# Optimization experiments

Measured on AMD Instinct MI355X. Metric: run time of the kernel, lower is better.

The kernel has to match this reference:

```python
import jax, jax.numpy as jnp
import numpy as np

EMBED_DIM = 768
NUM_HEADS = 12
HEAD_DIM = EMBED_DIM // NUM_HEADS
B, T = 2, 2048


def setup_inputs() -> dict:
    key = jax.random.key(0)
    ks = jax.random.split(key, 11)
    s = 1.0 / np.sqrt(EMBED_DIM)
    return {
        "query": jax.random.normal(ks[0], (B, T, EMBED_DIM), jnp.float32),
        "key_in": jax.random.normal(ks[1], (B, T, EMBED_DIM), jnp.float32),
        "value": jax.random.normal(ks[2], (B, T, EMBED_DIM), jnp.float32),
        "Wq": jax.random.uniform(ks[3], (EMBED_DIM, EMBED_DIM), jnp.float32, -s, s),
        "bq": jnp.zeros((EMBED_DIM,), jnp.float32),
        "Wk": jax.random.uniform(ks[4], (EMBED_DIM, EMBED_DIM), jnp.float32, -s, s),
        "bk": jnp.zeros((EMBED_DIM,), jnp.float32),
        "Wv": jax.random.uniform(ks[5], (EMBED_DIM, EMBED_DIM), jnp.float32, -s, s),
        "bv": jnp.zeros((EMBED_DIM,), jnp.float32),
        "Wo": jax.random.uniform(ks[6], (EMBED_DIM, EMBED_DIM), jnp.float32, -s, s),
        "bo": jnp.zeros((EMBED_DIM,), jnp.float32),
    }


def reference(query, key_in, value, Wq, bq, Wk, bk, Wv, bv, Wo, bo):
    b, t, _ = query.shape

    def split_heads(x):  # [B,T,E] -> [B,H,T,Dh]
        return x.reshape(b, t, NUM_HEADS, HEAD_DIM).transpose(0, 2, 1, 3)

    Q = split_heads(query @ Wq + bq)
    K = split_heads(key_in @ Wk + bk)
    V = split_heads(value @ Wv + bv)

    scores = jnp.einsum("bhqd,bhkd->bhqk", Q, K) / np.sqrt(HEAD_DIM).astype(np.float32)
    attn = jax.nn.softmax(scores, axis=-1)
    out = jnp.einsum("bhqk,bhkd->bhqd", attn, V)  # [B,H,T,Dh]
    out = out.transpose(0, 2, 1, 3).reshape(b, t, EMBED_DIM)
    return out @ Wo + bo
```

## Files before the change

kernel.cpp:

```cpp
#include <hip/hip_runtime.h>
#include <math.h>

typedef __attribute__((ext_vector_type(4))) float  floatx4;
typedef __attribute__((ext_vector_type(16))) float f32x16;
typedef __attribute__((ext_vector_type(8))) short  short8;
typedef __attribute__((ext_vector_type(4))) short  short4v;
typedef __attribute__((ext_vector_type(8))) __bf16 bf16x8;
typedef __attribute__((ext_vector_type(4))) unsigned int uint4v;

#define E_DIM 768
#define T_DIM 2048
#define N_B   2
#define N_H   12
#define H_D   64
#define M_TOT 4096

#define Q_SCALE 0.1803368801111204f

#if __has_builtin(__builtin_amdgcn_exp2f)
#define EXP2F(x) __builtin_amdgcn_exp2f(x)
#else
#define EXP2F(x) exp2f(x)
#endif
#if __has_builtin(__builtin_amdgcn_rcpf)
#define RCPF(x) __builtin_amdgcn_rcpf(x)
#else
#define RCPF(x) (1.0f / (x))
#endif

__device__ __forceinline__ unsigned short f32_to_bf16(float f) {
  unsigned int u = __float_as_uint(f);
  u += 0x7fffu + ((u >> 16) & 1u);
  return (unsigned short)(u >> 16);
}

__device__ __forceinline__ void lds_barrier() {
  asm volatile("s_waitcnt lgkmcnt(0)\n\ts_barrier" ::: "memory");
}

__device__ __forceinline__ void gload_lds16(const unsigned short* g, unsigned short* l) {
  __builtin_amdgcn_global_load_lds(
      (const __attribute__((address_space(1))) unsigned int*)(const void*)g,
      (__attribute__((address_space(3))) unsigned int*)(void*)l, 16, 0, 0);
}

__device__ __forceinline__ unsigned int cvtpk_bf16(float lo, float hi) {
  unsigned int r;
  asm("v_cvt_pk_bf16_f32 %0, %1, %2" : "=v"(r) : "v"(lo), "v"(hi));
  return r;
}

__device__ __forceinline__ void perml32_swap(unsigned int& a, unsigned int& b) {
  asm volatile("v_permlane32_swap_b32 %0, %1" : "+v"(a), "+v"(b));
}

__global__ __launch_bounds__(256) void convert_x(const float* __restrict__ q,
                                                 const float* __restrict__ k,
                                                 const float* __restrict__ v,
                                                 unsigned short* __restrict__ Xb) {
  const int z = blockIdx.y;
  const float* src = (z == 0) ? q : (z == 1) ? k : v;
  size_t idx = ((size_t)blockIdx.x * 256 + threadIdx.x) * 4;
  float4 val = *reinterpret_cast<const float4*>(&src[idx]);
  short4v o;
  o[0] = (short)f32_to_bf16(val.x);
  o[1] = (short)f32_to_bf16(val.y);
  o[2] = (short)f32_to_bf16(val.z);
  o[3] = (short)f32_to_bf16(val.w);
  *reinterpret_cast<short4v*>(&Xb[(size_t)z * M_TOT * E_DIM + idx]) = o;
}

__global__ __launch_bounds__(256) void transpose_w4(const float* __restrict__ W0,
                                                    const float* __restrict__ W1,
                                                    const float* __restrict__ W2,
                                                    const float* __restrict__ W3,
                                                    unsigned short* __restrict__ Wt) {
  __shared__ float tile[32][33];
  const int z = blockIdx.z;
  const float* W = (z == 0) ? W0 : (z == 1) ? W1 : (z == 2) ? W2 : W3;
  unsigned short* dst = Wt + (size_t)z * E_DIM * E_DIM;
  int k0 = blockIdx.x * 32, n0 = blockIdx.y * 32;
  int tx = threadIdx.x & 31, ty = threadIdx.x >> 5;
  for (int i = 0; i < 4; i++)
    tile[ty + i * 8][tx] = W[(size_t)(k0 + ty + i * 8) * E_DIM + n0 + tx];
  __syncthreads();
  for (int i = 0; i < 4; i++)
    dst[(size_t)(n0 + ty + i * 8) * E_DIM + k0 + tx] = f32_to_bf16(tile[tx][ty + i * 8]);
}

__global__ __launch_bounds__(256) void gemm_qkv(const unsigned short* __restrict__ Xb,
                                                const unsigned short* __restrict__ WtAll,
                                                const float* __restrict__ bq,
                                                const float* __restrict__ bk,
                                                const float* __restrict__ bv,
                                                unsigned short* __restrict__ outQKV) {
  __shared__ unsigned short As[128 * 32];
  __shared__ unsigned short Bs[128 * 32];

  const int z = blockIdx.z;
  const unsigned short* A = Xb + (size_t)z * M_TOT * E_DIM;
  const float* bias = (z == 0) ? bq : (z == 1) ? bk : bv;
  const unsigned short* W = WtAll + (size_t)z * E_DIM * E_DIM;
  unsigned short* out = outQKV + (size_t)z * M_TOT * E_DIM;
  const float scale = (z == 0) ? Q_SCALE : 1.0f;

  const int tid = threadIdx.x;
  const int lane = tid & 63, wv = tid >> 6;
  const int m15 = lane & 15, quad = lane >> 4;
  const int wm = (wv & 1) * 64, wn = (wv >> 1) * 64;
  const int m0 = blockIdx.x * 128, n0 = blockIdx.y * 128;

  floatx4 acc[4][4] = {};
  const int srow = lane >> 2, scol = (lane & 3) * 8;

  for (int k0 = 0; k0 < E_DIM; k0 += 32) {
    for (int cc = 0; cc < 2; cc++) {
      int c = wv * 2 + cc;
      gload_lds16(&A[(size_t)(m0 + c * 16 + srow) * E_DIM + k0 + scol], &As[c * 512]);
      gload_lds16(&W[(size_t)(n0 + c * 16 + srow) * E_DIM + k0 + scol], &Bs[c * 512]);
    }
    __syncthreads();
    bf16x8 af[4], bfr[4];
    for (int i = 0; i < 4; i++)
      af[i] = *reinterpret_cast<const bf16x8*>(&As[(wm + i * 16 + m15) * 32 + quad * 8]);
    for (int j = 0; j < 4; j++)
      bfr[j] = *reinterpret_cast<const bf16x8*>(&Bs[(wn + j * 16 + m15) * 32 + quad * 8]);
    for (int i = 0; i < 4; i++)
      for (int j = 0; j < 4; j++)
        acc[i][j] = __builtin_amdgcn_mfma_f32_16x16x32_bf16(af[i], bfr[j], acc[i][j], 0, 0, 0);
    __syncthreads();
  }

  for (int i = 0; i < 4; i++)
    for (int j = 0; j < 4; j++) {
      int gn = n0 + wn + j * 16 + m15;
      int h = gn >> 6, d = gn & 63;
      float bso = bias[gn];
      for (int r = 0; r < 4; r++) {
        int gm = m0 + wm + i * 16 + quad * 4 + r;
        int bb = gm >> 11, tt = gm & 2047;
        float v = (acc[i][j][r] + bso) * scale;
        out[(((size_t)bb * N_H + h) * T_DIM + tt) * H_D + d] = f32_to_bf16(v);
      }
    }
}

__global__ __launch_bounds__(256) void transpose_v(const unsigned short* __restrict__ Vg_all,
                                                   unsigned short* __restrict__ VT) {
  __shared__ unsigned short tile[64 * 72];
  const int t0 = blockIdx.x * 64, h = blockIdx.y, bb = blockIdx.z;
  const unsigned short* Vg = Vg_all + (((size_t)bb * N_H + h) * T_DIM) * H_D;
  unsigned short* VTh = VT + (((size_t)bb * N_H + h) * H_D) * T_DIM;
  const int tid = threadIdx.x;
  const int tloc = tid & 63, d0 = (tid >> 6) * 16;

  short8 r0 = *reinterpret_cast<const short8*>(&Vg[(size_t)(t0 + tloc) * H_D + d0]);
  short8 r1 = *reinterpret_cast<const short8*>(&Vg[(size_t)(t0 + tloc) * H_D + d0 + 8]);
#pragma unroll
  for (int j = 0; j < 8; j++) {
    tile[(d0 + j) * 72 + tloc] = (unsigned short)r0[j];
    tile[(d0 + 8 + j) * 72 + tloc] = (unsigned short)r1[j];
  }
  __syncthreads();
  const int d = tid >> 2, ts = (tid & 3) * 16;
  short8 w0 = *reinterpret_cast<const short8*>(&tile[d * 72 + ts]);
  short8 w1 = *reinterpret_cast<const short8*>(&tile[d * 72 + ts + 8]);
  *reinterpret_cast<short8*>(&VTh[(size_t)d * T_DIM + t0 + ts]) = w0;
  *reinterpret_cast<short8*>(&VTh[(size_t)d * T_DIM + t0 + ts + 8]) = w1;
}

__global__ __launch_bounds__(128) void attn(const unsigned short* __restrict__ QKV,
                                            const unsigned short* __restrict__ VT,
                                            unsigned short* __restrict__ ctx) {
  __shared__ unsigned short Ks[2][64 * 64];
  __shared__ unsigned short Vs[2][64 * 64];

  const int qt = blockIdx.x, h = blockIdx.y, bb = blockIdx.z;
  const size_t headoff = (((size_t)bb * N_H + h) * T_DIM) * H_D;
  const unsigned short* Qg = QKV + headoff;
  const unsigned short* Kg = QKV + (size_t)M_TOT * E_DIM + headoff;
  const unsigned short* VTg = VT + (((size_t)bb * N_H + h) * H_D) * T_DIM;

  const int tid = threadIdx.x;
  const int lane = tid & 63, wv = tid >> 6;
  const int l31 = lane & 31, hi = lane >> 5, l7 = lane & 7;
  const int q0 = qt * 64 + wv * 32;

  const int srow = lane >> 3;
  const int sslot = (lane & 7) ^ srow;
  const unsigned short* gK = Kg + (size_t)srow * H_D + sslot * 8;
  const unsigned short* gV = VTg + (size_t)srow * T_DIM + sslot * 8;

  bf16x8 aq[4];
#pragma unroll
  for (int c = 0; c < 4; c++)
    aq[c] = *reinterpret_cast<const bf16x8*>(&Qg[(size_t)(q0 + l31) * H_D + c * 16 + hi * 8]);

#pragma unroll
  for (int i = 0; i < 8; i++) {
    if (wv == 0) gload_lds16(gK + (size_t)(i * 8) * H_D, &Ks[0][i * 512]);
    else         gload_lds16(gV + (size_t)(i * 8) * T_DIM, &Vs[0][i * 512]);
  }
  if (wv == 0) {
#pragma unroll
    for (int i = 0; i < 8; i++)
      gload_lds16(gK + (size_t)(64 + i * 8) * H_D, &Ks[1][i * 512]);
  }
  asm volatile("s_waitcnt vmcnt(0)" ::: "memory");
  lds_barrier();

  f32x16 o0 = {}, o1 = {};
  float lacc = 0.f;
  bf16x8 pa0[2], pa1[2];

  auto QK = [&](const unsigned short* kb, f32x16& s0, f32x16& s1) {
#pragma unroll
    for (int c = 0; c < 4; c++) {
      const int slot = ((c << 1) | hi) ^ l7;
      bf16x8 k0 = *reinterpret_cast<const bf16x8*>(&kb[l31 * 64 + slot * 8]);
      bf16x8 k1 = *reinterpret_cast<const bf16x8*>(&kb[(32 + l31) * 64 + slot * 8]);
      s0 = __builtin_amdgcn_mfma_f32_32x32x16_bf16(k0, aq[c], s0, 0, 0, 0);
      s1 = __builtin_amdgcn_mfma_f32_32x32x16_bf16(k1, aq[c], s1, 0, 0, 0);
    }
  };
  auto PV = [&](const unsigned short* vb) {
#pragma unroll
    for (int cc = 0; cc < 2; cc++) {
      const int sl0 = ((cc << 1) | hi) ^ l7;
      const int sl1 = (4 + (cc << 1) + hi) ^ l7;
      bf16x8 v00 = *reinterpret_cast<const bf16x8*>(&vb[l31 * 64 + sl0 * 8]);
      bf16x8 v01 = *reinterpret_cast<const bf16x8*>(&vb[(32 + l31) * 64 + sl0 * 8]);
      bf16x8 v10 = *reinterpret_cast<const bf16x8*>(&vb[l31 * 64 + sl1 * 8]);
      bf16x8 v11 = *reinterpret_cast<const bf16x8*>(&vb[(32 + l31) * 64 + sl1 * 8]);
      o0 = __builtin_amdgcn_mfma_f32_32x32x16_bf16(pa0[cc], v00, o0, 0, 0, 0);
      o1 = __builtin_amdgcn_mfma_f32_32x32x16_bf16(pa0[cc], v01, o1, 0, 0, 0);
      o0 = __builtin_amdgcn_mfma_f32_32x32x16_bf16(pa1[cc], v10, o0, 0, 0, 0);
      o1 = __builtin_amdgcn_mfma_f32_32x32x16_bf16(pa1[cc], v11, o1, 0, 0, 0);
    }
  };
  auto PACK = [&](f32x16& s0, f32x16& s1) {
#pragma unroll
    for (int i = 0; i < 16; i++) { s0[i] = EXP2F(s0[i]); s1[i] = EXP2F(s1[i]); }
    float a0 = 0.f, a1 = 0.f, a2 = 0.f, a3 = 0.f;
#pragma unroll
    for (int i = 0; i < 16; i += 4) {
      a0 += s0[i]; a1 += s0[i + 1]; a2 += s0[i + 2]; a3 += s0[i + 3];
      a0 += s1[i]; a1 += s1[i + 1]; a2 += s1[i + 2]; a3 += s1[i + 3];
    }
    lacc += (a0 + a1) + (a2 + a3);
#pragma unroll
    for (int cc = 0; cc < 2; cc++) {
      {
        unsigned int x0 = cvtpk_bf16(s0[8 * cc + 0], s0[8 * cc + 1]);
        unsigned int x1 = cvtpk_bf16(s0[8 * cc + 2], s0[8 * cc + 3]);
        unsigned int y0 = cvtpk_bf16(s0[8 * cc + 4], s0[8 * cc + 5]);
        unsigned int y1 = cvtpk_bf16(s0[8 * cc + 6], s0[8 * cc + 7]);
        perml32_swap(x0, y0);
        perml32_swap(x1, y1);
        uint4v u; u[0] = x0; u[1] = x1; u[2] = y0; u[3] = y1;
        pa0[cc] = __builtin_bit_cast(bf16x8, u);
      }
      {
        unsigned int x0 = cvtpk_bf16(s1[8 * cc + 0], s1[8 * cc + 1]);
        unsigned int x1 = cvtpk_bf16(s1[8 * cc + 2], s1[8 * cc + 3]);
        unsigned int y0 = cvtpk_bf16(s1[8 * cc + 4], s1[8 * cc + 5]);
        unsigned int y1 = cvtpk_bf16(s1[8 * cc + 6], s1[8 * cc + 7]);
        perml32_swap(x0, y0);
        perml32_swap(x1, y1);
        uint4v u; u[0] = x0; u[1] = x1; u[2] = y0; u[3] = y1;
        pa1[cc] = __builtin_bit_cast(bf16x8, u);
      }
    }
  };

  {
    f32x16 s0 = {}, s1 = {};
    __builtin_amdgcn_s_setprio(1);
    QK(Ks[0], s0, s1);
    __builtin_amdgcn_s_setprio(0);
    lds_barrier();
#pragma unroll
    for (int i = 0; i < 8; i++) {
      if (wv == 0) gload_lds16(gK + (size_t)(128 + i * 8) * H_D, &Ks[0][i * 512]);
      else         gload_lds16(gV + (size_t)(i * 8) * T_DIM + 64, &Vs[1][i * 512]);
    }
    PACK(s0, s1);
    asm volatile("s_waitcnt vmcnt(8)" ::: "memory");
    lds_barrier();
  }

  for (int kt = 1; kt <= 30; ++kt) {
    f32x16 s0 = {}, s1 = {};
    __builtin_amdgcn_s_setprio(1);
    QK(Ks[kt & 1], s0, s1);
    PV(Vs[(kt - 1) & 1]);
    __builtin_amdgcn_s_setprio(0);
    lds_barrier();
    if (wv == 0) {
      if (kt < 30) {
        const int nt = kt + 2;
#pragma unroll
        for (int i = 0; i < 8; i++)
          gload_lds16(gK + (size_t)(nt * 64 + i * 8) * H_D, &Ks[kt & 1][i * 512]);
      }
    } else {
      const int nt = kt + 1;
#pragma unroll
      for (int i = 0; i < 8; i++)
        gload_lds16(gV + (size_t)(i * 8) * T_DIM + nt * 64, &Vs[nt & 1][i * 512]);
    }
    PACK(s0, s1);
    if (kt == 30) asm volatile("s_waitcnt vmcnt(0)" ::: "memory");
    else          asm volatile("s_waitcnt vmcnt(8)" ::: "memory");
    lds_barrier();
  }

  {
    f32x16 s0 = {}, s1 = {};
    __builtin_amdgcn_s_setprio(1);
    QK(Ks[1], s0, s1);
    PV(Vs[0]);
    __builtin_amdgcn_s_setprio(0);
    PACK(s0, s1);
    __builtin_amdgcn_s_setprio(1);
    PV(Vs[1]);
    __builtin_amdgcn_s_setprio(0);
  }

  float ltot = lacc + __shfl_xor(lacc, 32, 64);
  float rl = RCPF(ltot);
  const size_t obase = ((size_t)bb * T_DIM + q0) * E_DIM + (size_t)h * H_D;
#pragma unroll
  for (int r = 0; r < 16; r++) {
    const int qrow = (r & 3) + 8 * (r >> 2) + 4 * hi;
    float rq = __shfl(rl, qrow, 64);
    ctx[obase + (size_t)qrow * E_DIM + l31]      = f32_to_bf16(o0[r] * rq);
    ctx[obase + (size_t)qrow * E_DIM + 32 + l31] = f32_to_bf16(o1[r] * rq);
  }
}

__global__ __launch_bounds__(256) void gemm_out(const unsigned short* __restrict__ Actx,
                                                const unsigned short* __restrict__ Wt,
                                                const float* __restrict__ bias,
                                                float* __restrict__ out) {
  __shared__ unsigned short As[64 * 32];
  __shared__ unsigned short Bs[128 * 32];

  const int tid = threadIdx.x;
  const int lane = tid & 63, wv = tid >> 6;
  const int m15 = lane & 15, quad = lane >> 4;
  const int wm = (wv & 1) * 32, wn = (wv >> 1) * 64;
  const int m0 = blockIdx.x * 64, n0 = blockIdx.y * 128;

  floatx4 acc[2][4] = {};
  const int srow = lane >> 2, scol = (lane & 3) * 8;

  for (int k0 = 0; k0 < E_DIM; k0 += 32) {
    gload_lds16(&Actx[(size_t)(m0 + wv * 16 + srow) * E_DIM + k0 + scol], &As[wv * 512]);
    for (int cc = 0; cc < 2; cc++) {
      int c = wv * 2 + cc;
      gload_lds16(&Wt[(size_t)(n0 + c * 16 + srow) * E_DIM + k0 + scol], &Bs[c * 512]);
    }
    __syncthreads();
    bf16x8 af[2], bfr[4];
    for (int i = 0; i < 2; i++)
      af[i] = *reinterpret_cast<const bf16x8*>(&As[(wm + i * 16 + m15) * 32 + quad * 8]);
    for (int j = 0; j < 4; j++)
      bfr[j] = *reinterpret_cast<const bf16x8*>(&Bs[(wn + j * 16 + m15) * 32 + quad * 8]);
    for (int i = 0; i < 2; i++)
      for (int j = 0; j < 4; j++)
        acc[i][j] = __builtin_amdgcn_mfma_f32_16x16x32_bf16(af[i], bfr[j], acc[i][j], 0, 0, 0);
    __syncthreads();
  }

  for (int i = 0; i < 2; i++)
    for (int j = 0; j < 4; j++) {
      int gn = n0 + wn + j * 16 + m15;
      float bso = bias[gn];
      for (int r = 0; r < 4; r++) {
        int gm = m0 + wm + i * 16 + quad * 4 + r;
        out[(size_t)gm * E_DIM + gn] = acc[i][j][r] + bso;
      }
    }
}

extern "C" void kernel_launch(void* const* d_in, const int* in_sizes, int n_in,
                              void* d_out, int out_size, void* d_ws, size_t ws_size,
                              hipStream_t stream) {
  const float* query  = (const float*)d_in[0];
  const float* key_in = (const float*)d_in[1];
  const float* value  = (const float*)d_in[2];
  const float* Wq = (const float*)d_in[3];
  const float* bq = (const float*)d_in[4];
  const float* Wk = (const float*)d_in[5];
  const float* bk = (const float*)d_in[6];
  const float* Wv = (const float*)d_in[7];
  const float* bv = (const float*)d_in[8];
  const float* Wo = (const float*)d_in[9];
  const float* bo = (const float*)d_in[10];
  float* out = (float*)d_out;

  unsigned short* ws  = (unsigned short*)d_ws;
  unsigned short* Wt  = ws;
  unsigned short* Xb  = Wt + (size_t)4 * E_DIM * E_DIM;
  unsigned short* QKV = Xb + (size_t)3 * M_TOT * E_DIM;
  unsigned short* VT  = QKV + (size_t)3 * M_TOT * E_DIM;
  unsigned short* ctx = VT + (size_t)N_B * N_H * H_D * T_DIM;

  dim3 tb(256);
  convert_x<<<dim3(M_TOT * E_DIM / 1024, 3), tb, 0, stream>>>(query, key_in, value, Xb);
  transpose_w4<<<dim3(24, 24, 4), tb, 0, stream>>>(Wq, Wk, Wv, Wo, Wt);

  gemm_qkv<<<dim3(32, 6, 3), tb, 0, stream>>>(Xb, Wt, bq, bk, bv, QKV);
  transpose_v<<<dim3(32, 12, 2), tb, 0, stream>>>(QKV + (size_t)2 * M_TOT * E_DIM, VT);
  attn<<<dim3(32, 12, 2), dim3(128), 0, stream>>>(QKV, VT, ctx);
  gemm_out<<<dim3(64, 6), tb, 0, stream>>>(ctx, Wt + (size_t)3 * E_DIM * E_DIM, bo, out);
  (void)in_sizes; (void)n_in; (void)out_size; (void)ws_size;
}
```

Before: 194.6 us.

## Process 64 query rows per single-wave attention block, drop LDS barriers

```diff
diff --git a/kernel.cpp b/kernel.cpp
--- a/kernel.cpp
+++ b/kernel.cpp
@@ -169,9 +169,9 @@
   *reinterpret_cast<short8*>(&VTh[(size_t)d * T_DIM + t0 + ts + 8]) = w1;
 }
 
-__global__ __launch_bounds__(128) void attn(const unsigned short* __restrict__ QKV,
-                                            const unsigned short* __restrict__ VT,
-                                            unsigned short* __restrict__ ctx) {
+__global__ __launch_bounds__(64, 1) void attn(const unsigned short* __restrict__ QKV,
+                                              const unsigned short* __restrict__ VT,
+                                              unsigned short* __restrict__ ctx) {
   __shared__ unsigned short Ks[2][64 * 64];
   __shared__ unsigned short Vs[2][64 * 64];
 
@@ -181,46 +181,48 @@
   const unsigned short* Kg = QKV + (size_t)M_TOT * E_DIM + headoff;
   const unsigned short* VTg = VT + (((size_t)bb * N_H + h) * H_D) * T_DIM;
 
-  const int tid = threadIdx.x;
-  const int lane = tid & 63, wv = tid >> 6;
+  const int lane = threadIdx.x;
   const int l31 = lane & 31, hi = lane >> 5, l7 = lane & 7;
-  const int q0 = qt * 64 + wv * 32;
+  const int q0 = qt * 64;
 
   const int srow = lane >> 3;
   const int sslot = (lane & 7) ^ srow;
   const unsigned short* gK = Kg + (size_t)srow * H_D + sslot * 8;
   const unsigned short* gV = VTg + (size_t)srow * T_DIM + sslot * 8;
 
-  bf16x8 aq[4];
-#pragma unroll
-  for (int c = 0; c < 4; c++)
-    aq[c] = *reinterpret_cast<const bf16x8*>(&Qg[(size_t)(q0 + l31) * H_D + c * 16 + hi * 8]);
+  bf16x8 aqA[4], aqB[4];
+#pragma unroll
+  for (int c = 0; c < 4; c++) {
+    aqA[c] = *reinterpret_cast<const bf16x8*>(&Qg[(size_t)(q0 + l31) * H_D + c * 16 + hi * 8]);
+    aqB[c] = *reinterpret_cast<const bf16x8*>(&Qg[(size_t)(q0 + 32 + l31) * H_D + c * 16 + hi * 8]);
+  }
 
 #pragma unroll
   for (int i = 0; i < 8; i++) {
-    if (wv == 0) gload_lds16(gK + (size_t)(i * 8) * H_D, &Ks[0][i * 512]);
-    else         gload_lds16(gV + (size_t)(i * 8) * T_DIM, &Vs[0][i * 512]);
-  }
-  if (wv == 0) {
-#pragma unroll
-    for (int i = 0; i < 8; i++)
-      gload_lds16(gK + (size_t)(64 + i * 8) * H_D, &Ks[1][i * 512]);
-  }
-  asm volatile("s_waitcnt vmcnt(0)" ::: "memory");
-  lds_barrier();
-
-  f32x16 o0 = {}, o1 = {};
-  float lacc = 0.f;
-  bf16x8 pa0[2], pa1[2];
-
-  auto QK = [&](const unsigned short* kb, f32x16& s0, f32x16& s1) {
+    gload_lds16(gK + (size_t)(i * 8) * H_D, &Ks[0][i * 512]);
+    gload_lds16(gV + (size_t)(i * 8) * T_DIM, &Vs[0][i * 512]);
+  }
+#pragma unroll
+  for (int i = 0; i < 8; i++) {
+    gload_lds16(gK + (size_t)(64 + i * 8) * H_D, &Ks[1][i * 512]);
+    gload_lds16(gV + (size_t)(i * 8) * T_DIM + 64, &Vs[1][i * 512]);
+  }
+  asm volatile("s_waitcnt vmcnt(16)" ::: "memory");
+
+  f32x16 oA0 = {}, oA1 = {}, oB0 = {}, oB1 = {};
+  float laccA = 0.f, laccB = 0.f;
+  bf16x8 paA0[2], paA1[2], paB0[2], paB1[2];
+
+  auto QK = [&](const unsigned short* kb, f32x16& a0, f32x16& a1, f32x16& b0, f32x16& b1) {
 #pragma unroll
     for (int c = 0; c < 4; c++) {
       const int slot = ((c << 1) | hi) ^ l7;
       bf16x8 k0 = *reinterpret_cast<const bf16x8*>(&kb[l31 * 64 + slot * 8]);
       bf16x8 k1 = *reinterpret_cast<const bf16x8*>(&kb[(32 + l31) * 64 + slot * 8]);
-      s0 = __builtin_amdgcn_mfma_f32_32x32x16_bf16(k0, aq[c], s0, 0, 0, 0);
-      s1 = __builtin_amdgcn_mfma_f32_32x32x16_bf16(k1, aq[c], s1, 0, 0, 0);
+      a0 = __builtin_amdgcn_mfma_f32_32x32x16_bf16(k0, aqA[c], a0, 0, 0, 0);
+      a1 = __builtin_amdgcn_mfma_f32_32x32x16_bf16(k1, aqA[c], a1, 0, 0, 0);
+      b0 = __builtin_amdgcn_mfma_f32_32x32x16_bf16(k0, aqB[c], b0, 0, 0, 0);
+      b1 = __builtin_amdgcn_mfma_f32_32x32x16_bf16(k1, aqB[c], b1, 0, 0, 0);
     }
   };
   auto PV = [&](const unsigned short* vb) {
@@ -232,13 +234,17 @@
       bf16x8 v01 = *reinterpret_cast<const bf16x8*>(&vb[(32 + l31) * 64 + sl0 * 8]);
       bf16x8 v10 = *reinterpret_cast<const bf16x8*>(&vb[l31 * 64 + sl1 * 8]);
       bf16x8 v11 = *reinterpret_cast<const bf16x8*>(&vb[(32 + l31) * 64 + sl1 * 8]);
-      o0 = __builtin_amdgcn_mfma_f32_32x32x16_bf16(pa0[cc], v00, o0, 0, 0, 0);
-      o1 = __builtin_amdgcn_mfma_f32_32x32x16_bf16(pa0[cc], v01, o1, 0, 0, 0);
-      o0 = __builtin_amdgcn_mfma_f32_32x32x16_bf16(pa1[cc], v10, o0, 0, 0, 0);
-      o1 = __builtin_amdgcn_mfma_f32_32x32x16_bf16(pa1[cc], v11, o1, 0, 0, 0);
+      oA0 = __builtin_amdgcn_mfma_f32_32x32x16_bf16(paA0[cc], v00, oA0, 0, 0, 0);
+      oA1 = __builtin_amdgcn_mfma_f32_32x32x16_bf16(paA0[cc], v01, oA1, 0, 0, 0);
+      oA0 = __builtin_amdgcn_mfma_f32_32x32x16_bf16(paA1[cc], v10, oA0, 0, 0, 0);
+      oA1 = __builtin_amdgcn_mfma_f32_32x32x16_bf16(paA1[cc], v11, oA1, 0, 0, 0);
+      oB0 = __builtin_amdgcn_mfma_f32_32x32x16_bf16(paB0[cc], v00, oB0, 0, 0, 0);
+      oB1 = __builtin_amdgcn_mfma_f32_32x32x16_bf16(paB0[cc], v01, oB1, 0, 0, 0);
+      oB0 = __builtin_amdgcn_mfma_f32_32x32x16_bf16(paB1[cc], v10, oB0, 0, 0, 0);
+      oB1 = __builtin_amdgcn_mfma_f32_32x32x16_bf16(paB1[cc], v11, oB1, 0, 0, 0);
     }
   };
-  auto PACK = [&](f32x16& s0, f32x16& s1) {
+  auto PACK1 = [&](f32x16& s0, f32x16& s1, float& lacc, bf16x8* pl, bf16x8* ph) {
 #pragma unroll
     for (int i = 0; i < 16; i++) { s0[i] = EXP2F(s0[i]); s1[i] = EXP2F(s1[i]); }
     float a0 = 0.f, a1 = 0.f, a2 = 0.f, a3 = 0.f;
@@ -258,7 +264,7 @@
         perml32_swap(x0, y0);
         perml32_swap(x1, y1);
         uint4v u; u[0] = x0; u[1] = x1; u[2] = y0; u[3] = y1;
-        pa0[cc] = __builtin_bit_cast(bf16x8, u);
+        pl[cc] = __builtin_bit_cast(bf16x8, u);
       }
       {
         unsigned int x0 = cvtpk_bf16(s1[8 * cc + 0], s1[8 * cc + 1]);
@@ -268,74 +274,78 @@
         perml32_swap(x0, y0);
         perml32_swap(x1, y1);
         uint4v u; u[0] = x0; u[1] = x1; u[2] = y0; u[3] = y1;
-        pa1[cc] = __builtin_bit_cast(bf16x8, u);
+        ph[cc] = __builtin_bit_cast(bf16x8, u);
       }
     }
   };
 
   {
-    f32x16 s0 = {}, s1 = {};
+    f32x16 sA0 = {}, sA1 = {}, sB0 = {}, sB1 = {};
     __builtin_amdgcn_s_setprio(1);
-    QK(Ks[0], s0, s1);
+    QK(Ks[0], sA0, sA1, sB0, sB1);
     __builtin_amdgcn_s_setprio(0);
-    lds_barrier();
-#pragma unroll
-    for (int i = 0; i < 8; i++) {
-      if (wv == 0) gload_lds16(gK + (size_t)(128 + i * 8) * H_D, &Ks[0][i * 512]);
-      else         gload_lds16(gV + (size_t)(i * 8) * T_DIM + 64, &Vs[1][i * 512]);
-    }
-    PACK(s0, s1);
+    asm volatile("s_waitcnt lgkmcnt(0)" ::: "memory");
+#pragma unroll
+    for (int i = 0; i < 8; i++)
+      gload_lds16(gK + (size_t)(128 + i * 8) * H_D, &Ks[0][i * 512]);
+    PACK1(sA0, sA1, laccA, paA0, paA1);
+    PACK1(sB0, sB1, laccB, paB0, paB1);
     asm volatile("s_waitcnt vmcnt(8)" ::: "memory");
-    lds_barrier();
   }
 
   for (int kt = 1; kt <= 30; ++kt) {
-    f32x16 s0 = {}, s1 = {};
+    f32x16 sA0 = {}, sA1 = {}, sB0 = {}, sB1 = {};
     __builtin_amdgcn_s_setprio(1);
-    QK(Ks[kt & 1], s0, s1);
+    QK(Ks[kt & 1], sA0, sA1, sB0, sB1);
     PV(Vs[(kt - 1) & 1]);
     __builtin_amdgcn_s_setprio(0);
-    lds_barrier();
-    if (wv == 0) {
-      if (kt < 30) {
-        const int nt = kt + 2;
-#pragma unroll
-        for (int i = 0; i < 8; i++)
-          gload_lds16(gK + (size_t)(nt * 64 + i * 8) * H_D, &Ks[kt & 1][i * 512]);
-      }
-    } else {
-      const int nt = kt + 1;
+    asm volatile("s_waitcnt lgkmcnt(0)" ::: "memory");
+    if (kt < 30) {
+      const int nk = kt + 2;
 #pragma unroll
       for (int i = 0; i < 8; i++)
-        gload_lds16(gV + (size_t)(i * 8) * T_DIM + nt * 64, &Vs[nt & 1][i * 512]);
-    }
-    PACK(s0, s1);
-    if (kt == 30) asm volatile("s_waitcnt vmcnt(0)" ::: "memory");
-    else          asm volatile("s_waitcnt vmcnt(8)" ::: "memory");
-    lds_barrier();
+        gload_lds16(gK + (size_t)(nk * 64 + i * 8) * H_D, &Ks[kt & 1][i * 512]);
+    }
+    {
+      const int nv = kt + 1;
+#pragma unroll
+      for (int i = 0; i < 8; i++)
+        gload_lds16(gV + (size_t)(i * 8) * T_DIM + nv * 64, &Vs[nv & 1][i * 512]);
+    }
+    PACK1(sA0, sA1, laccA, paA0, paA1);
+    PACK1(sB0, sB1, laccB, paB0, paB1);
+    if (kt < 30) asm volatile("s_waitcnt vmcnt(16)" ::: "memory");
+    else         asm volatile("s_waitcnt vmcnt(8)" ::: "memory");
   }
 
   {
-    f32x16 s0 = {}, s1 = {};
+    f32x16 sA0 = {}, sA1 = {}, sB0 = {}, sB1 = {};
     __builtin_amdgcn_s_setprio(1);
-    QK(Ks[1], s0, s1);
+    QK(Ks[1], sA0, sA1, sB0, sB1);
     PV(Vs[0]);
     __builtin_amdgcn_s_setprio(0);
-    PACK(s0, s1);
+    PACK1(sA0, sA1, laccA, paA0, paA1);
+    PACK1(sB0, sB1, laccB, paB0, paB1);
+    asm volatile("s_waitcnt vmcnt(0)" ::: "memory");
     __builtin_amdgcn_s_setprio(1);
     PV(Vs[1]);
     __builtin_amdgcn_s_setprio(0);
   }
 
-  float ltot = lacc + __shfl_xor(lacc, 32, 64);
-  float rl = RCPF(ltot);
+  float ltA = laccA + __shfl_xor(laccA, 32, 64);
+  float rlA = RCPF(ltA);
+  float ltB = laccB + __shfl_xor(laccB, 32, 64);
+  float rlB = RCPF(ltB);
   const size_t obase = ((size_t)bb * T_DIM + q0) * E_DIM + (size_t)h * H_D;
 #pragma unroll
   for (int r = 0; r < 16; r++) {
-    const int qrow = (r & 3) + 8 * (r >> 2) + 4 * hi;
-    float rq = __shfl(rl, qrow, 64);
-    ctx[obase + (size_t)qrow * E_DIM + l31]      = f32_to_bf16(o0[r] * rq);
-    ctx[obase + (size_t)qrow * E_DIM + 32 + l31] = f32_to_bf16(o1[r] * rq);
+    const int qr = (r & 3) + 8 * (r >> 2) + 4 * hi;
+    float ra = __shfl(rlA, qr, 64);
+    ctx[obase + (size_t)qr * E_DIM + l31]      = f32_to_bf16(oA0[r] * ra);
+    ctx[obase + (size_t)qr * E_DIM + 32 + l31] = f32_to_bf16(oA1[r] * ra);
+    float rb = __shfl(rlB, qr, 64);
+    ctx[obase + (size_t)(32 + qr) * E_DIM + l31]      = f32_to_bf16(oB0[r] * rb);
+    ctx[obase + (size_t)(32 + qr) * E_DIM + 32 + l31] = f32_to_bf16(oB1[r] * rb);
   }
 }
 
@@ -413,7 +423,7 @@
 
   gemm_qkv<<<dim3(32, 6, 3), tb, 0, stream>>>(Xb, Wt, bq, bk, bv, QKV);
   transpose_v<<<dim3(32, 12, 2), tb, 0, stream>>>(QKV + (size_t)2 * M_TOT * E_DIM, VT);
-  attn<<<dim3(32, 12, 2), dim3(128), 0, stream>>>(QKV, VT, ctx);
+  attn<<<dim3(32, 12, 2), dim3(64), 0, stream>>>(QKV, VT, ctx);
   gemm_out<<<dim3(64, 6), tb, 0, stream>>>(ctx, Wt + (size_t)3 * E_DIM * E_DIM, bo, out);
   (void)in_sizes; (void)n_in; (void)out_size; (void)ws_size;
 }
```

Result: no change. 198.1 us (+1.8%).

## Run attention as single-wave blocks without barriers; merge prep kernels into one launch

Applied to the files above, without the earlier changes.

```diff
diff --git a/kernel.cpp b/kernel.cpp
--- a/kernel.cpp
+++ b/kernel.cpp
@@ -34,10 +34,6 @@
   return (unsigned short)(u >> 16);
 }
 
-__device__ __forceinline__ void lds_barrier() {
-  asm volatile("s_waitcnt lgkmcnt(0)\n\ts_barrier" ::: "memory");
-}
-
 __device__ __forceinline__ void gload_lds16(const unsigned short* g, unsigned short* l) {
   __builtin_amdgcn_global_load_lds(
       (const __attribute__((address_space(1))) unsigned int*)(const void*)g,
@@ -54,38 +50,41 @@
   asm volatile("v_permlane32_swap_b32 %0, %1" : "+v"(a), "+v"(b));
 }
 
-__global__ __launch_bounds__(256) void convert_x(const float* __restrict__ q,
-                                                 const float* __restrict__ k,
-                                                 const float* __restrict__ v,
-                                                 unsigned short* __restrict__ Xb) {
-  const int z = blockIdx.y;
-  const float* src = (z == 0) ? q : (z == 1) ? k : v;
-  size_t idx = ((size_t)blockIdx.x * 256 + threadIdx.x) * 4;
-  float4 val = *reinterpret_cast<const float4*>(&src[idx]);
-  short4v o;
-  o[0] = (short)f32_to_bf16(val.x);
-  o[1] = (short)f32_to_bf16(val.y);
-  o[2] = (short)f32_to_bf16(val.z);
-  o[3] = (short)f32_to_bf16(val.w);
-  *reinterpret_cast<short4v*>(&Xb[(size_t)z * M_TOT * E_DIM + idx]) = o;
-}
-
-__global__ __launch_bounds__(256) void transpose_w4(const float* __restrict__ W0,
-                                                    const float* __restrict__ W1,
-                                                    const float* __restrict__ W2,
-                                                    const float* __restrict__ W3,
-                                                    unsigned short* __restrict__ Wt) {
+__global__ __launch_bounds__(256) void prep(const float* __restrict__ q,
+                                            const float* __restrict__ k,
+                                            const float* __restrict__ v,
+                                            const float* __restrict__ W0,
+                                            const float* __restrict__ W1,
+                                            const float* __restrict__ W2,
+                                            const float* __restrict__ W3,
+                                            unsigned short* __restrict__ Xb,
+                                            unsigned short* __restrict__ Wt) {
   __shared__ float tile[32][33];
-  const int z = blockIdx.z;
-  const float* W = (z == 0) ? W0 : (z == 1) ? W1 : (z == 2) ? W2 : W3;
-  unsigned short* dst = Wt + (size_t)z * E_DIM * E_DIM;
-  int k0 = blockIdx.x * 32, n0 = blockIdx.y * 32;
-  int tx = threadIdx.x & 31, ty = threadIdx.x >> 5;
-  for (int i = 0; i < 4; i++)
-    tile[ty + i * 8][tx] = W[(size_t)(k0 + ty + i * 8) * E_DIM + n0 + tx];
-  __syncthreads();
-  for (int i = 0; i < 4; i++)
-    dst[(size_t)(n0 + ty + i * 8) * E_DIM + k0 + tx] = f32_to_bf16(tile[tx][ty + i * 8]);
+  const int b = blockIdx.x, tid = threadIdx.x;
+  if (b < 9216) {
+    const int z = b / 3072, bx = b - z * 3072;
+    const float* src = (z == 0) ? q : (z == 1) ? k : v;
+    size_t idx = ((size_t)bx * 256 + tid) * 4;
+    float4 val = *reinterpret_cast<const float4*>(&src[idx]);
+    short4v o;
+    o[0] = (short)f32_to_bf16(val.x);
+    o[1] = (short)f32_to_bf16(val.y);
+    o[2] = (short)f32_to_bf16(val.z);
+    o[3] = (short)f32_to_bf16(val.w);
+    *reinterpret_cast<short4v*>(&Xb[(size_t)z * M_TOT * E_DIM + idx]) = o;
+  } else {
+    const int t = b - 9216;
+    const int z = t / 576, rem = t - z * 576;
+    const int k0 = (rem / 24) * 32, n0 = (rem % 24) * 32;
+    const float* W = (z == 0) ? W0 : (z == 1) ? W1 : (z == 2) ? W2 : W3;
+    unsigned short* dst = Wt + (size_t)z * E_DIM * E_DIM;
+    const int tx = tid & 31, ty = tid >> 5;
+    for (int i = 0; i < 4; i++)
+      tile[ty + i * 8][tx] = W[(size_t)(k0 + ty + i * 8) * E_DIM + n0 + tx];
+    __syncthreads();
+    for (int i = 0; i < 4; i++)
+      dst[(size_t)(n0 + ty + i * 8) * E_DIM + k0 + tx] = f32_to_bf16(tile[tx][ty + i * 8]);
+  }
 }
 
 __global__ __launch_bounds__(256) void gemm_qkv(const unsigned short* __restrict__ Xb,
@@ -169,9 +168,9 @@
   *reinterpret_cast<short8*>(&VTh[(size_t)d * T_DIM + t0 + ts + 8]) = w1;
 }
 
-__global__ __launch_bounds__(128) void attn(const unsigned short* __restrict__ QKV,
-                                            const unsigned short* __restrict__ VT,
-                                            unsigned short* __restrict__ ctx) {
+__global__ __launch_bounds__(64, 1) void attn(const unsigned short* __restrict__ QKV,
+                                              const unsigned short* __restrict__ VT,
+                                              unsigned short* __restrict__ ctx) {
   __shared__ unsigned short Ks[2][64 * 64];
   __shared__ unsigned short Vs[2][64 * 64];
 
@@ -181,10 +180,9 @@
   const unsigned short* Kg = QKV + (size_t)M_TOT * E_DIM + headoff;
   const unsigned short* VTg = VT + (((size_t)bb * N_H + h) * H_D) * T_DIM;
 
-  const int tid = threadIdx.x;
-  const int lane = tid & 63, wv = tid >> 6;
+  const int lane = threadIdx.x;
   const int l31 = lane & 31, hi = lane >> 5, l7 = lane & 7;
-  const int q0 = qt * 64 + wv * 32;
+  const int q0 = qt * 32;
 
   const int srow = lane >> 3;
   const int sslot = (lane & 7) ^ srow;
@@ -198,16 +196,15 @@
 
 #pragma unroll
   for (int i = 0; i < 8; i++) {
-    if (wv == 0) gload_lds16(gK + (size_t)(i * 8) * H_D, &Ks[0][i * 512]);
-    else         gload_lds16(gV + (size_t)(i * 8) * T_DIM, &Vs[0][i * 512]);
-  }
-  if (wv == 0) {
-#pragma unroll
-    for (int i = 0; i < 8; i++)
-      gload_lds16(gK + (size_t)(64 + i * 8) * H_D, &Ks[1][i * 512]);
-  }
-  asm volatile("s_waitcnt vmcnt(0)" ::: "memory");
-  lds_barrier();
+    gload_lds16(gK + (size_t)(i * 8) * H_D, &Ks[0][i * 512]);
+    gload_lds16(gV + (size_t)(i * 8) * T_DIM, &Vs[0][i * 512]);
+  }
+#pragma unroll
+  for (int i = 0; i < 8; i++) {
+    gload_lds16(gK + (size_t)(64 + i * 8) * H_D, &Ks[1][i * 512]);
+    gload_lds16(gV + (size_t)(i * 8) * T_DIM + 64, &Vs[1][i * 512]);
+  }
+  asm volatile("s_waitcnt vmcnt(16)" ::: "memory");
 
   f32x16 o0 = {}, o1 = {};
   float lacc = 0.f;
@@ -238,7 +235,7 @@
       o1 = __builtin_amdgcn_mfma_f32_32x32x16_bf16(pa1[cc], v11, o1, 0, 0, 0);
     }
   };
-  auto PACK = [&](f32x16& s0, f32x16& s1) {
+  auto PACK1 = [&](f32x16& s0, f32x16& s1) {
 #pragma unroll
     for (int i = 0; i < 16; i++) { s0[i] = EXP2F(s0[i]); s1[i] = EXP2F(s1[i]); }
     float a0 = 0.f, a1 = 0.f, a2 = 0.f, a3 = 0.f;
@@ -278,15 +275,12 @@
     __builtin_amdgcn_s_setprio(1);
     QK(Ks[0], s0, s1);
     __builtin_amdgcn_s_setprio(0);
-    lds_barrier();
-#pragma unroll
-    for (int i = 0; i < 8; i++) {
-      if (wv == 0) gload_lds16(gK + (size_t)(128 + i * 8) * H_D, &Ks[0][i * 512]);
-      else         gload_lds16(gV + (size_t)(i * 8) * T_DIM + 64, &Vs[1][i * 512]);
-    }
-    PACK(s0, s1);
+    asm volatile("s_waitcnt lgkmcnt(0)" ::: "memory");
+#pragma unroll
+    for (int i = 0; i < 8; i++)
+      gload_lds16(gK + (size_t)(128 + i * 8) * H_D, &Ks[0][i * 512]);
+    PACK1(s0, s1);
     asm volatile("s_waitcnt vmcnt(8)" ::: "memory");
-    lds_barrier();
   }
 
   for (int kt = 1; kt <= 30; ++kt) {
@@ -295,24 +289,22 @@
     QK(Ks[kt & 1], s0, s1);
     PV(Vs[(kt - 1) & 1]);
     __builtin_amdgcn_s_setprio(0);
-    lds_barrier();
-    if (wv == 0) {
-      if (kt < 30) {
-        const int nt = kt + 2;
-#pragma unroll
-        for (int i = 0; i < 8; i++)
-          gload_lds16(gK + (size_t)(nt * 64 + i * 8) * H_D, &Ks[kt & 1][i * 512]);
-      }
-    } else {
-      const int nt = kt + 1;
+    asm volatile("s_waitcnt lgkmcnt(0)" ::: "memory");
+    if (kt < 30) {
+      const int nk = kt + 2;
 #pragma unroll
       for (int i = 0; i < 8; i++)
-        gload_lds16(gV + (size_t)(i * 8) * T_DIM + nt * 64, &Vs[nt & 1][i * 512]);
-    }
-    PACK(s0, s1);
-    if (kt == 30) asm volatile("s_waitcnt vmcnt(0)" ::: "memory");
-    else          asm volatile("s_waitcnt vmcnt(8)" ::: "memory");
-    lds_barrier();
+        gload_lds16(gK + (size_t)(nk * 64 + i * 8) * H_D, &Ks[kt & 1][i * 512]);
+    }
+    {
+      const int nv = kt + 1;
+#pragma unroll
+      for (int i = 0; i < 8; i++)
+        gload_lds16(gV + (size_t)(i * 8) * T_DIM + nv * 64, &Vs[nv & 1][i * 512]);
+    }
+    PACK1(s0, s1);
+    if (kt < 30) asm volatile("s_waitcnt vmcnt(16)" ::: "memory");
+    else         asm volatile("s_waitcnt vmcnt(8)" ::: "memory");
   }
 
   {
@@ -321,7 +313,8 @@
     QK(Ks[1], s0, s1);
     PV(Vs[0]);
     __builtin_amdgcn_s_setprio(0);
-    PACK(s0, s1);
+    PACK1(s0, s1);
+    asm volatile("s_waitcnt vmcnt(0)" ::: "memory");
     __builtin_amdgcn_s_setprio(1);
     PV(Vs[1]);
     __builtin_amdgcn_s_setprio(0);
@@ -332,10 +325,10 @@
   const size_t obase = ((size_t)bb * T_DIM + q0) * E_DIM + (size_t)h * H_D;
 #pragma unroll
   for (int r = 0; r < 16; r++) {
-    const int qrow = (r & 3) + 8 * (r >> 2) + 4 * hi;
-    float rq = __shfl(rl, qrow, 64);
-    ctx[obase + (size_t)qrow * E_DIM + l31]      = f32_to_bf16(o0[r] * rq);
-    ctx[obase + (size_t)qrow * E_DIM + 32 + l31] = f32_to_bf16(o1[r] * rq);
+    const int qr = (r & 3) + 8 * (r >> 2) + 4 * hi;
+    float rq = __shfl(rl, qr, 64);
+    ctx[obase + (size_t)qr * E_DIM + l31]      = f32_to_bf16(o0[r] * rq);
+    ctx[obase + (size_t)qr * E_DIM + 32 + l31] = f32_to_bf16(o1[r] * rq);
   }
 }
 
@@ -408,12 +401,10 @@
   unsigned short* ctx = VT + (size_t)N_B * N_H * H_D * T_DIM;
 
   dim3 tb(256);
-  convert_x<<<dim3(M_TOT * E_DIM / 1024, 3), tb, 0, stream>>>(query, key_in, value, Xb);
-  transpose_w4<<<dim3(24, 24, 4), tb, 0, stream>>>(Wq, Wk, Wv, Wo, Wt);
-
+  prep<<<dim3(11520), tb, 0, stream>>>(query, key_in, value, Wq, Wk, Wv, Wo, Xb, Wt);
   gemm_qkv<<<dim3(32, 6, 3), tb, 0, stream>>>(Xb, Wt, bq, bk, bv, QKV);
   transpose_v<<<dim3(32, 12, 2), tb, 0, stream>>>(QKV + (size_t)2 * M_TOT * E_DIM, VT);
-  attn<<<dim3(32, 12, 2), dim3(128), 0, stream>>>(QKV, VT, ctx);
+  attn<<<dim3(64, 12, 2), dim3(64), 0, stream>>>(QKV, VT, ctx);
   gemm_out<<<dim3(64, 6), tb, 0, stream>>>(ctx, Wt + (size_t)3 * E_DIM * E_DIM, bo, out);
   (void)in_sizes; (void)n_in; (void)out_size; (void)ws_size;
 }
```

After: 217.9 us. 1.12x slower.
